# Performance work log

Hardware: AMD Instinct MI355X
Metric: run time of the kernel (lower is better)

Reference implementation:

```python
import jax, jax.numpy as jnp
import numpy as np
import math

WS = (8, 8)        # window_size for context (2D)
HEADS = 8


def _attend(q, k, v, h):
    # q: (Bw, Nq, inner), k/v: (Bw, Nk, inner)
    Bw, Nq, inner = q.shape
    d = inner // h
    q = q.reshape(Bw, Nq, h, d)
    k = k.reshape(Bw, -1, h, d)
    v = v.reshape(Bw, -1, h, d)
    scores = jnp.einsum('bqhd,bkhd->bhqk', q, k) * (d ** -0.5)
    attn = jax.nn.softmax(scores, axis=-1)
    out = jnp.einsum('bhqk,bkhd->bqhd', attn, v)
    return out.reshape(Bw, Nq, inner)


def reference(x, context, W_q, W_k, W_v, W_out, b_out):
    B, C, T, H, W = x.shape
    H_, W_ = context.shape[-2], context.shape[-1]
    ws = WS
    assert H_ * W_ > ws[0] * ws[1] and H * W >= ws[0] * ws[1]  # window branch
    # pad context to multiple of window_size (no-op for chosen shapes)
    pad_r_2d = (-W_) % ws[1]
    pad_b_2d = (-H_) % ws[0]
    context = jnp.pad(context, ((0, 0), (0, 0), (0, pad_b_2d), (0, pad_r_2d)))
    # scaled window size for the (smaller) 3D query tensor
    ws_ = (math.ceil(float(ws[0]) * H / H_), math.ceil(float(ws[1]) * W / W_))
    pad_r_3d = (-W) % ws_[1]
    pad_b_3d = (-H) % ws_[0]
    x = jnp.pad(x, ((0, 0), (0, 0), (0, 0), (0, pad_b_3d), (0, pad_r_3d)))
    Hp, Wp = x.shape[-2], x.shape[-1]
    Hc, Wc = context.shape[-2], context.shape[-1]
    # window partition: context (B,C,Hc,Wc) -> (B*h*w, ws0*ws1, C)
    hc, wc = Hc // ws[0], Wc // ws[1]
    ctx = context.reshape(B, C, hc, ws[0], wc, ws[1])
    ctx = ctx.transpose(0, 2, 4, 3, 5, 1).reshape(B * hc * wc, ws[0] * ws[1], C)
    # window partition: x (B,C,T,Hp,Wp) -> (B*h*w, T*ws_0*ws_1, C)
    hg, wg = Hp // ws_[0], Wp // ws_[1]
    xw = x.reshape(B, C, T, hg, ws_[0], wg, ws_[1])
    xw = xw.transpose(0, 3, 5, 2, 4, 6, 1).reshape(B * hg * wg, T * ws_[0] * ws_[1], C)
    # QKV projections (no bias: qkv_bias=False, to_k always bias-free)
    q = xw @ W_q
    k = ctx @ W_k
    v = ctx @ W_v
    out = _attend(q, k, v, HEADS)  # (Bw, Nq, inner)
    inner = out.shape[-1]
    # window reverse -> (B, inner, T, Hp, Wp)
    out = out.reshape(B, hg, wg, T, ws_[0], ws_[1], inner)
    out = out.transpose(0, 6, 3, 1, 4, 2, 5).reshape(B, inner, T, Hp, Wp)
    out = out[:, :, :, :H, :W]
    # b c t h w -> b (t h w) c
    out = out.transpose(0, 2, 3, 4, 1).reshape(B, T * H * W, inner)
    return out @ W_out + b_out


def setup_inputs() -> dict:
    key = jax.random.key(0)
    ks = jax.random.split(key, 7)
    D = 512
    s = 0.02
    return {
        'x': jax.random.normal(ks[0], (4, D, 4, 32, 32), jnp.float32),
        'context': jax.random.normal(ks[1], (4, D, 128, 128), jnp.float32),
        'W_q': jax.random.normal(ks[2], (D, D), jnp.float32) * s,
        'W_k': jax.random.normal(ks[3], (D, D), jnp.float32) * s,
        'W_v': jax.random.normal(ks[4], (D, D), jnp.float32) * s,
        'W_out': jax.random.normal(ks[5], (D, D), jnp.float32) * s,
        'b_out': jnp.zeros((D,), jnp.float32),
    }
```

## Files before the change

kernel.cpp:

```cpp
#include <hip/hip_runtime.h>
#include <hip/hip_bf16.h>

typedef unsigned short u16;
typedef unsigned int u32;
typedef __attribute__((ext_vector_type(4))) float f32x4;
typedef __attribute__((ext_vector_type(4))) u16 u16x4;
typedef __attribute__((ext_vector_type(8))) u16 u16x8;
typedef __attribute__((ext_vector_type(8))) short s16x8;

__device__ __forceinline__ u16 f2bf(float f) {
    union { float f; u32 u; } v; v.f = f;
    u32 r = v.u + 0x7FFFu + ((v.u >> 16) & 1u);
    return (u16)(r >> 16);
}

__device__ __forceinline__ void gl_lds16(const u16* g, u16* l) {
    __builtin_amdgcn_global_load_lds(
        (const __attribute__((address_space(1))) unsigned int*)(const void*)g,
        (__attribute__((address_space(3))) unsigned int*)(void*)l, 16, 0, 0);
}

__global__ __launch_bounds__(256) void wtrans_kernel(
    const float* __restrict__ w0, const float* __restrict__ w1,
    const float* __restrict__ w2, const float* __restrict__ w3,
    u16* __restrict__ dst) {
    __shared__ float t[64][65];
    int wsel = blockIdx.x >> 6;
    int tile = blockIdx.x & 63;
    int j0 = (tile >> 3) * 64, c0 = (tile & 7) * 64;
    const float* src = wsel == 0 ? w0 : wsel == 1 ? w1 : wsel == 2 ? w2 : w3;
    u16* out = dst + (long)wsel * 512 * 512;
    int tj = threadIdx.x & 63;
    int ti = threadIdx.x >> 6;
#pragma unroll
    for (int p = 0; p < 16; ++p) {
        int row = p * 4 + ti;
        t[row][tj] = src[(long)(c0 + row) * 512 + j0 + tj];
    }
    __syncthreads();
#pragma unroll
    for (int p = 0; p < 16; ++p) {
        int jl = p * 4 + ti;
        out[(long)(j0 + jl) * 512 + c0 + tj] = f2bf(t[tj][jl]);
    }
}

__global__ __launch_bounds__(256) void permx_kernel(const float* __restrict__ x, u16* __restrict__ Aq) {
    __shared__ u16 t[64][36];
    int bid = blockIdx.x;
    int cb = bid & 7; bid >>= 3;
    int y  = bid & 31; bid >>= 5;
    int tt = bid & 3; bid >>= 2;
    int b  = bid;
    int tid = threadIdx.x;
    long ibase = ((long)(b * 512 + cb * 64) * 4 + tt) * 1024 + y * 32;
#pragma unroll
    for (int p = 0; p < 2; ++p) {
        int task = p * 256 + tid;
        int cc = task >> 3, xl = (task & 7) * 4;
        float4 v = *(const float4*)&x[ibase + (long)cc * 4096 + xl];
        u16x4 o = {f2bf(v.x), f2bf(v.y), f2bf(v.z), f2bf(v.w)};
        *(u16x4*)&t[cc][xl] = o;
    }
    __syncthreads();
    {
        int xx = tid >> 3, j = tid & 7;
        u16x8 o;
#pragma unroll
        for (int i = 0; i < 8; ++i) o[i] = t[j * 8 + i][xx];
        int row = b * 4096 + (y >> 1) * 256 + (xx >> 1) * 16 + tt * 4 + (y & 1) * 2 + (xx & 1);
        *(u16x8*)&Aq[(long)row * 512 + cb * 64 + j * 8] = o;
    }
}

__global__ __launch_bounds__(256) void permc_kernel(const float* __restrict__ ctx, u16* __restrict__ Actx) {
    __shared__ u16 t[64][68];
    int bid = blockIdx.x;
    int cb = bid & 7; bid >>= 3;
    int xb = bid & 1; bid >>= 1;
    int y  = bid & 127; bid >>= 7;
    int b  = bid;
    int tid = threadIdx.x;
    long ibase = ((long)(b * 512 + cb * 64) * 128 + y) * 128 + xb * 64;
#pragma unroll
    for (int p = 0; p < 4; ++p) {
        int task = p * 256 + tid;
        int cc = task >> 4, xl = (task & 15) * 4;
        float4 v = *(const float4*)&ctx[ibase + (long)cc * 16384 + xl];
        u16x4 o = {f2bf(v.x), f2bf(v.y), f2bf(v.z), f2bf(v.w)};
        *(u16x4*)&t[cc][xl] = o;
    }
    __syncthreads();
#pragma unroll
    for (int p = 0; p < 2; ++p) {
        int task = p * 256 + tid;
        int xx = task >> 3, j = task & 7;
        u16x8 o;
#pragma unroll
        for (int i = 0; i < 8; ++i) o[i] = t[j * 8 + i][xx];
        int xg = xb * 64 + xx;
        int row = b * 16384 + (y >> 3) * 1024 + (xg >> 3) * 64 + (y & 7) * 8 + (xg & 7);
        *(u16x8*)&Actx[(long)row * 512 + cb * 64 + j * 8] = o;
    }
}

template <int FINAL>
__global__ __launch_bounds__(256, 4) void gemm128_kernel(
    const u16* __restrict__ A, const u16* __restrict__ Bt,
    u16* __restrict__ Cb, float* __restrict__ Cf, const float* __restrict__ bias) {
    __shared__ u16 As[1024 * 8];
    __shared__ u16 Bs[1024 * 8];
    int tid = threadIdx.x;
    int lane = tid & 63;
    int w = tid >> 6;
    int wm = w >> 1, wn = w & 1;
    int bid = blockIdx.x;
    int wg = (bid & 7) * 64 + (bid >> 3);
    int m0 = (wg >> 2) * 128;
    int n0 = (wg & 3) * 128;

    const f32x4 z = {0.f, 0.f, 0.f, 0.f};
    f32x4 acc[4][4];
#pragma unroll
    for (int i = 0; i < 4; ++i)
#pragma unroll
        for (int j = 0; j < 4; ++j) acc[i][j] = z;

    int aoff[4], boff[4], lb[4];
#pragma unroll
    for (int i = 0; i < 4; ++i) {
        int s = i * 256 + tid;
        int row = s >> 3;
        int cb = (s & 7) ^ (row & 7);
        aoff[i] = (m0 + row) * 512 + cb * 8;
        boff[i] = (n0 + row) * 512 + cb * 8;
        lb[i] = (i * 256 + w * 64) * 8;
    }
    int la = lane & 15, lg = lane >> 4;
    for (int ks = 0; ks < 8; ++ks) {
        int ko = ks * 64;
#pragma unroll
        for (int i = 0; i < 4; ++i) {
            gl_lds16(&A[aoff[i] + ko], &As[lb[i]]);
            gl_lds16(&Bt[boff[i] + ko], &Bs[lb[i]]);
        }
        __syncthreads();
#pragma unroll
        for (int kk = 0; kk < 2; ++kk) {
            int cb = kk * 4 + lg;
            s16x8 af[4], bfr[4];
#pragma unroll
            for (int mt = 0; mt < 4; ++mt) {
                int r = wm * 64 + mt * 16 + la;
                af[mt] = *(const s16x8*)&As[r * 64 + ((cb ^ (r & 7)) * 8)];
            }
#pragma unroll
            for (int nt = 0; nt < 4; ++nt) {
                int c = wn * 64 + nt * 16 + la;
                bfr[nt] = *(const s16x8*)&Bs[c * 64 + ((cb ^ (c & 7)) * 8)];
            }
#pragma unroll
            for (int mt = 0; mt < 4; ++mt)
#pragma unroll
                for (int nt = 0; nt < 4; ++nt)
                    acc[mt][nt] = __builtin_amdgcn_mfma_f32_16x16x32_bf16(af[mt], bfr[nt], acc[mt][nt], 0, 0, 0);
        }
        __syncthreads();
    }
#pragma unroll
    for (int mt = 0; mt < 4; ++mt) {
#pragma unroll
        for (int nt = 0; nt < 4; ++nt) {
            int col = n0 + wn * 64 + nt * 16 + la;
#pragma unroll
            for (int rr = 0; rr < 4; ++rr) {
                int r = m0 + wm * 64 + mt * 16 + lg * 4 + rr;
                float v = acc[mt][nt][rr];
                if (FINAL) {
                    int bb = r >> 12, hg = (r >> 8) & 15, wgx = (r >> 4) & 15;
                    int tt = (r >> 2) & 3, rr0 = (r >> 1) & 1, cc0 = r & 1;
                    int tok = bb * 4096 + tt * 1024 + (hg * 2 + rr0) * 32 + wgx * 2 + cc0;
                    Cf[(long)tok * 512 + col] = v + bias[col];
                } else {
                    Cb[(long)r * 512 + col] = f2bf(v);
                }
            }
        }
    }
}

__global__ __launch_bounds__(512, 2) void gemmkv256_kernel(
    const u16* __restrict__ A, const u16* __restrict__ B, u16* __restrict__ C) {
    __shared__ u16 lds[2][2][16384];
    int tid = threadIdx.x;
    int lane = tid & 63;
    int w = tid >> 6;
    int wm = w >> 2, wn = w & 3;
    int la = lane & 15, lg = lane >> 4;
    int bid = blockIdx.x;
    int wg = (bid & 7) * 128 + (bid >> 3);
    int m0 = (wg >> 2) * 256;
    int n0 = (wg & 3) * 256;

    const f32x4 z = {0.f, 0.f, 0.f, 0.f};
    f32x4 acc[8][4];
#pragma unroll
    for (int i = 0; i < 8; ++i)
#pragma unroll
        for (int j = 0; j < 4; ++j) acc[i][j] = z;

    int aoff[4], boff[4], lsl[4];
#pragma unroll
    for (int i = 0; i < 4; ++i) {
        int s = i * 512 + tid;
        int row = s >> 3;
        int cb = (s & 7) ^ (row & 7);
        aoff[i] = (m0 + row) * 512 + cb * 8;
        boff[i] = (n0 + row) * 512 + cb * 8;
        lsl[i] = (i * 512 + w * 64) * 8;
    }

    auto STAGE = [&](int t, int buf) {
#pragma unroll
        for (int i = 0; i < 4; ++i) {
            gl_lds16(&A[aoff[i] + t * 64], &lds[buf][0][lsl[i]]);
            gl_lds16(&B[boff[i] + t * 64], &lds[buf][1][lsl[i]]);
        }
    };
    auto COMPUTE = [&](int buf) {
        const u16* Ab = lds[buf][0];
        const u16* Bb = lds[buf][1];
#pragma unroll
        for (int kk = 0; kk < 2; ++kk) {
            int cb = kk * 4 + lg;
            s16x8 af[8], bfr[4];
#pragma unroll
            for (int mt = 0; mt < 8; ++mt) {
                int r = wm * 128 + mt * 16 + la;
                af[mt] = *(const s16x8*)&Ab[r * 64 + ((cb ^ (r & 7)) * 8)];
            }
#pragma unroll
            for (int nt = 0; nt < 4; ++nt) {
                int c = wn * 64 + nt * 16 + la;
                bfr[nt] = *(const s16x8*)&Bb[c * 64 + ((cb ^ (c & 7)) * 8)];
            }
            __builtin_amdgcn_s_setprio(1);
#pragma unroll
            for (int mt = 0; mt < 8; ++mt)
#pragma unroll
                for (int nt = 0; nt < 4; ++nt)
                    acc[mt][nt] = __builtin_amdgcn_mfma_f32_16x16x32_bf16(af[mt], bfr[nt], acc[mt][nt], 0, 0, 0);
            __builtin_amdgcn_s_setprio(0);
        }
    };

    STAGE(0, 0);
    STAGE(1, 1);
    asm volatile("s_waitcnt vmcnt(8)" ::: "memory");
    __builtin_amdgcn_s_barrier();
    asm volatile("" ::: "memory");

#pragma unroll
    for (int t = 0; t < 8; ++t) {
        COMPUTE(t & 1);
        if (t < 6) {
            asm volatile("" ::: "memory");
            __builtin_amdgcn_s_barrier();
            STAGE(t + 2, t & 1);
            asm volatile("s_waitcnt vmcnt(8)" ::: "memory");
            __builtin_amdgcn_s_barrier();
            asm volatile("" ::: "memory");
        } else if (t == 6) {
            asm volatile("s_waitcnt vmcnt(0)" ::: "memory");
            __builtin_amdgcn_s_barrier();
            asm volatile("" ::: "memory");
        }
    }

#pragma unroll
    for (int mt = 0; mt < 8; ++mt) {
#pragma unroll
        for (int nt = 0; nt < 4; ++nt) {
            int col = n0 + wn * 64 + nt * 16 + la;
#pragma unroll
            for (int rr = 0; rr < 4; ++rr) {
                int r = m0 + wm * 128 + mt * 16 + lg * 4 + rr;
                C[(long)r * 1024 + col] = f2bf(acc[mt][nt][rr]);
            }
        }
    }
}

__global__ __launch_bounds__(64) void attn_kernel(
    const u16* __restrict__ Q, const u16* __restrict__ KV, u16* __restrict__ O) {
    __shared__ u16 P[16 * 104];
    int bid = blockIdx.x;
    int wg = (bid & 7) * 1024 + (bid >> 3);
    int win = wg >> 3;
    int h = wg & 7;
    int lane = threadIdx.x;
    int la = lane & 15, lg = lane >> 4;
    const u16* Qb = Q + (long)win * 16 * 512 + h * 64;
    const u16* Kb = KV + (long)win * 64 * 1024 + h * 64;
    const u16* Vb = KV + (long)win * 64 * 1024 + 512 + h * 64;

    s16x8 qf[2];
#pragma unroll
    for (int kk = 0; kk < 2; ++kk)
        qf[kk] = *(const s16x8*)&Qb[la * 512 + kk * 32 + lg * 8];

    const f32x4 z = {0.f, 0.f, 0.f, 0.f};
    f32x4 st[4];
#pragma unroll
    for (int rt = 0; rt < 4; ++rt) st[rt] = z;
#pragma unroll
    for (int rt = 0; rt < 4; ++rt)
#pragma unroll
        for (int kk = 0; kk < 2; ++kk) {
            s16x8 kf = *(const s16x8*)&Kb[(rt * 16 + la) * 1024 + kk * 32 + lg * 8];
            st[rt] = __builtin_amdgcn_mfma_f32_16x16x32_bf16(kf, qf[kk], st[rt], 0, 0, 0);
        }
    float mloc = -1e30f;
#pragma unroll
    for (int rt = 0; rt < 4; ++rt)
#pragma unroll
        for (int rr = 0; rr < 4; ++rr) {
            st[rt][rr] *= 0.125f;
            mloc = fmaxf(mloc, st[rt][rr]);
        }
    mloc = fmaxf(mloc, __shfl_xor(mloc, 16));
    mloc = fmaxf(mloc, __shfl_xor(mloc, 32));
    float p[4][4];
    float sloc = 0.f;
#pragma unroll
    for (int rt = 0; rt < 4; ++rt)
#pragma unroll
        for (int rr = 0; rr < 4; ++rr) {
            p[rt][rr] = __expf(st[rt][rr] - mloc);
            sloc += p[rt][rr];
        }
    sloc += __shfl_xor(sloc, 16);
    sloc += __shfl_xor(sloc, 32);
    float inv = 1.0f / sloc;
#pragma unroll
    for (int rt = 0; rt < 4; ++rt)
#pragma unroll
        for (int rr = 0; rr < 4; ++rr)
            P[la * 104 + rt * 16 + lg * 4 + rr] = f2bf(p[rt][rr] * inv);
    __syncthreads();

    f32x4 od[4];
#pragma unroll
    for (int dt = 0; dt < 4; ++dt) od[dt] = z;
#pragma unroll
    for (int kk2 = 0; kk2 < 2; ++kk2) {
        s16x8 pa = *(const s16x8*)&P[la * 104 + kk2 * 32 + lg * 8];
#pragma unroll
        for (int dt = 0; dt < 4; ++dt) {
            s16x8 vb;
#pragma unroll
            for (int j = 0; j < 8; ++j)
                vb[j] = (short)Vb[(long)(kk2 * 32 + lg * 8 + j) * 1024 + dt * 16 + la];
            od[dt] = __builtin_amdgcn_mfma_f32_16x16x32_bf16(pa, vb, od[dt], 0, 0, 0);
        }
    }
    u16* Ob = O + (long)win * 16 * 512 + h * 64;
#pragma unroll
    for (int dt = 0; dt < 4; ++dt)
#pragma unroll
        for (int rr = 0; rr < 4; ++rr)
            Ob[(long)(lg * 4 + rr) * 512 + dt * 16 + la] = f2bf(od[dt][rr]);
}

__global__ void sentinel_kernel(float* out) {
    if (threadIdx.x == 0 && blockIdx.x == 0) out[0] = -12345.0f;
}

extern "C" void kernel_launch(void* const* d_in, const int* in_sizes, int n_in,
                              void* d_out, int out_size, void* d_ws, size_t ws_size,
                              hipStream_t stream) {
    const float* x   = (const float*)d_in[0];
    const float* ctx = (const float*)d_in[1];
    const float* Wq  = (const float*)d_in[2];
    const float* Wk  = (const float*)d_in[3];
    const float* Wv  = (const float*)d_in[4];
    const float* Wo  = (const float*)d_in[5];
    const float* bo  = (const float*)d_in[6];
    float* out = (float*)d_out;

    u16* wsb  = (u16*)d_ws;
    u16* WT   = wsb;
    u16* Aq   = WT + 4l * 262144;
    u16* Actx = Aq + 8388608l;
    u16* Qb   = Actx + 33554432l;
    u16* KVb  = Qb + 8388608l;
    u16* Ob   = KVb + 67108864l;
    size_t need = (size_t)(126877696l) * 2;
    if (ws_size < need) {
        sentinel_kernel<<<1, 64, 0, stream>>>(out);
        return;
    }

    wtrans_kernel<<<256, 256, 0, stream>>>(Wq, Wk, Wv, Wo, WT);
    permx_kernel<<<4096, 256, 0, stream>>>(x, Aq);
    permc_kernel<<<8192, 256, 0, stream>>>(ctx, Actx);
    gemm128_kernel<0><<<512, 256, 0, stream>>>(Aq, WT, Qb, nullptr, nullptr);
    gemmkv256_kernel<<<1024, 512, 0, stream>>>(Actx, WT + 262144l, KVb);
    attn_kernel<<<8192, 64, 0, stream>>>(Qb, KVb, Ob);
    gemm128_kernel<1><<<512, 256, 0, stream>>>(Ob, WT + 3l * 262144, nullptr, out, bo);
}
```

Baseline: 206.0 us.

## Interleave global-to-LDS prefetch with MFMA phases in GEMM main loop

The GEMM main loop is split into four compute phases over half-tiles of M and halves of K. B fragments are held in registers and reused across phases, so the next K-tile's global-to-LDS loads can be issued mid-iteration into the buffer being consumed, once its data is no longer needed. This aims to overlap memory traffic with MFMA work rather than staging after the full compute. It adds more s_barrier and sched_barrier points per iteration, and correctness depends on exact ordering between overwriting the LDS buffer and the last reads from it.

After: 203.1 us. No clear change (-1.4%).

```diff
diff --git a/kernel.cpp b/kernel.cpp
--- a/kernel.cpp
+++ b/kernel.cpp
@@ -220,53 +220,128 @@
         lsl[i] = (i * 512 + w * 64) * 8;
     }
 
-    auto STAGE = [&](int t, int buf) {
-#pragma unroll
-        for (int i = 0; i < 4; ++i) {
-            gl_lds16(&A[aoff[i] + t * 64], &lds[buf][0][lsl[i]]);
-            gl_lds16(&B[boff[i] + t * 64], &lds[buf][1][lsl[i]]);
-        }
-    };
-    auto COMPUTE = [&](int buf) {
-        const u16* Ab = lds[buf][0];
-        const u16* Bb = lds[buf][1];
-#pragma unroll
-        for (int kk = 0; kk < 2; ++kk) {
-            int cb = kk * 4 + lg;
-            s16x8 af[8], bfr[4];
-#pragma unroll
-            for (int mt = 0; mt < 8; ++mt) {
-                int r = wm * 128 + mt * 16 + la;
-                af[mt] = *(const s16x8*)&Ab[r * 64 + ((cb ^ (r & 7)) * 8)];
-            }
-#pragma unroll
-            for (int nt = 0; nt < 4; ++nt) {
-                int c = wn * 64 + nt * 16 + la;
-                bfr[nt] = *(const s16x8*)&Bb[c * 64 + ((cb ^ (c & 7)) * 8)];
-            }
-            __builtin_amdgcn_s_setprio(1);
-#pragma unroll
-            for (int mt = 0; mt < 8; ++mt)
-#pragma unroll
-                for (int nt = 0; nt < 4; ++nt)
-                    acc[mt][nt] = __builtin_amdgcn_mfma_f32_16x16x32_bf16(af[mt], bfr[nt], acc[mt][nt], 0, 0, 0);
-            __builtin_amdgcn_s_setprio(0);
-        }
-    };
-
-    STAGE(0, 0);
-    STAGE(1, 1);
+    s16x8 bfr[4][2];
+
+#pragma unroll
+    for (int i = 0; i < 4; ++i) {
+        gl_lds16(&A[aoff[i]], &lds[0][0][lsl[i]]);
+        gl_lds16(&B[boff[i]], &lds[0][1][lsl[i]]);
+    }
+#pragma unroll
+    for (int i = 0; i < 4; ++i) {
+        gl_lds16(&A[aoff[i] + 64], &lds[1][0][lsl[i]]);
+        gl_lds16(&B[boff[i] + 64], &lds[1][1][lsl[i]]);
+    }
     asm volatile("s_waitcnt vmcnt(8)" ::: "memory");
     __builtin_amdgcn_s_barrier();
     asm volatile("" ::: "memory");
 
 #pragma unroll
     for (int t = 0; t < 8; ++t) {
-        COMPUTE(t & 1);
+        int buf = t & 1;
+        const u16* Ab = lds[buf][0];
+        const u16* Bb = lds[buf][1];
+        int ko2 = (t + 2) * 64;
+
+        {
+            int cb = lg;
+            s16x8 af[4];
+#pragma unroll
+            for (int mt = 0; mt < 4; ++mt) {
+                int r = wm * 128 + mt * 16 + la;
+                af[mt] = *(const s16x8*)&Ab[r * 64 + ((cb ^ (r & 7)) * 8)];
+            }
+#pragma unroll
+            for (int nt = 0; nt < 4; ++nt) {
+                int c = wn * 64 + nt * 16 + la;
+                bfr[nt][0] = *(const s16x8*)&Bb[c * 64 + ((cb ^ (c & 7)) * 8)];
+            }
+            __builtin_amdgcn_s_barrier();
+            __builtin_amdgcn_s_setprio(1);
+#pragma unroll
+            for (int mt = 0; mt < 4; ++mt)
+#pragma unroll
+                for (int nt = 0; nt < 4; ++nt)
+                    acc[mt][nt] = __builtin_amdgcn_mfma_f32_16x16x32_bf16(af[mt], bfr[nt][0], acc[mt][nt], 0, 0, 0);
+            __builtin_amdgcn_s_setprio(0);
+            __builtin_amdgcn_sched_barrier(0);
+            __builtin_amdgcn_s_barrier();
+        }
+        {
+            int cb = 4 + lg;
+            s16x8 af[4];
+#pragma unroll
+            for (int mt = 0; mt < 4; ++mt) {
+                int r = wm * 128 + mt * 16 + la;
+                af[mt] = *(const s16x8*)&Ab[r * 64 + ((cb ^ (r & 7)) * 8)];
+            }
+#pragma unroll
+            for (int nt = 0; nt < 4; ++nt) {
+                int c = wn * 64 + nt * 16 + la;
+                bfr[nt][1] = *(const s16x8*)&Bb[c * 64 + ((cb ^ (c & 7)) * 8)];
+            }
+            __builtin_amdgcn_s_barrier();
+            __builtin_amdgcn_s_setprio(1);
+#pragma unroll
+            for (int mt = 0; mt < 4; ++mt)
+#pragma unroll
+                for (int nt = 0; nt < 4; ++nt)
+                    acc[mt][nt] = __builtin_amdgcn_mfma_f32_16x16x32_bf16(af[mt], bfr[nt][1], acc[mt][nt], 0, 0, 0);
+            __builtin_amdgcn_s_setprio(0);
+            __builtin_amdgcn_sched_barrier(0);
+            __builtin_amdgcn_s_barrier();
+        }
+        {
+            int cb = 4 + lg;
+            s16x8 af[4];
+#pragma unroll
+            for (int mt = 0; mt < 4; ++mt) {
+                int r = wm * 128 + 64 + mt * 16 + la;
+                af[mt] = *(const s16x8*)&Ab[r * 64 + ((cb ^ (r & 7)) * 8)];
+            }
+            if (t < 6) {
+                gl_lds16(&B[boff[0] + ko2], &lds[buf][1][lsl[0]]);
+                gl_lds16(&B[boff[1] + ko2], &lds[buf][1][lsl[1]]);
+                gl_lds16(&A[aoff[0] + ko2], &lds[buf][0][lsl[0]]);
+            }
+            __builtin_amdgcn_s_barrier();
+            __builtin_amdgcn_s_setprio(1);
+#pragma unroll
+            for (int mt = 0; mt < 4; ++mt)
+#pragma unroll
+                for (int nt = 0; nt < 4; ++nt)
+                    acc[4 + mt][nt] = __builtin_amdgcn_mfma_f32_16x16x32_bf16(af[mt], bfr[nt][1], acc[4 + mt][nt], 0, 0, 0);
+            __builtin_amdgcn_s_setprio(0);
+            __builtin_amdgcn_sched_barrier(0);
+            __builtin_amdgcn_s_barrier();
+        }
+        {
+            int cb = lg;
+            s16x8 af[4];
+#pragma unroll
+            for (int mt = 0; mt < 4; ++mt) {
+                int r = wm * 128 + 64 + mt * 16 + la;
+                af[mt] = *(const s16x8*)&Ab[r * 64 + ((cb ^ (r & 7)) * 8)];
+            }
+            if (t < 6) {
+                gl_lds16(&B[boff[2] + ko2], &lds[buf][1][lsl[2]]);
+                gl_lds16(&B[boff[3] + ko2], &lds[buf][1][lsl[3]]);
+                gl_lds16(&A[aoff[2] + ko2], &lds[buf][0][lsl[2]]);
+            }
+            __builtin_amdgcn_s_barrier();
+            __builtin_amdgcn_s_setprio(1);
+#pragma unroll
+            for (int mt = 0; mt < 4; ++mt)
+#pragma unroll
+                for (int nt = 0; nt < 4; ++nt)
+                    acc[4 + mt][nt] = __builtin_amdgcn_mfma_f32_16x16x32_bf16(af[mt], bfr[nt][0], acc[4 + mt][nt], 0, 0, 0);
+            __builtin_amdgcn_s_setprio(0);
+            __builtin_amdgcn_sched_barrier(0);
+            __builtin_amdgcn_s_barrier();
+        }
         if (t < 6) {
-            asm volatile("" ::: "memory");
-            __builtin_amdgcn_s_barrier();
-            STAGE(t + 2, t & 1);
+            gl_lds16(&A[aoff[1] + ko2], &lds[buf][0][lsl[1]]);
+            gl_lds16(&A[aoff[3] + ko2], &lds[buf][0][lsl[3]]);
             asm volatile("s_waitcnt vmcnt(8)" ::: "memory");
             __builtin_amdgcn_s_barrier();
             asm volatile("" ::: "memory");
```
